# Kernel tuning notes

Hardware: AMD Instinct MI355X
Metric: run time of the kernel (lower is better)

Reference implementation:

```python
import jax, jax.numpy as jnp
import numpy as np

T, D, H = 2048, 2048, 16
DH = D // H


def setup_inputs() -> dict:
    key = jax.random.key(0)
    ks = jax.random.split(key, 9)
    s = 1.0 / np.sqrt(D)
    return {
        "x": jax.random.normal(ks[0], (T, D), jnp.float32),
        "Wq": jax.random.normal(ks[1], (D, D), jnp.float32) * s,
        "bq": jax.random.normal(ks[2], (D,), jnp.float32) * s,
        "Wk": jax.random.normal(ks[3], (D, D), jnp.float32) * s,
        "bk": jax.random.normal(ks[4], (D,), jnp.float32) * s,
        "Wv": jax.random.normal(ks[5], (D, D), jnp.float32) * s,
        "bv": jax.random.normal(ks[6], (D,), jnp.float32) * s,
        "Wo": jax.random.normal(ks[7], (D, D), jnp.float32) * s,
        "bo": jax.random.normal(ks[8], (D,), jnp.float32) * s,
    }


def reference(x, Wq, bq, Wk, bk, Wv, bv, Wo, bo):
    # torch Linear: y = x @ W.T + b; weights are [out, in]
    Q = (x @ Wq.T + bq).reshape(T, H, DH).transpose(1, 0, 2)  # [H, T, dh]
    K = (x @ Wk.T + bk).reshape(T, H, DH).transpose(1, 0, 2)
    V = (x @ Wv.T + bv).reshape(T, H, DH).transpose(1, 0, 2)
    scores = jnp.einsum("htd,hsd->hts", Q, K) / jnp.sqrt(jnp.float32(DH))
    causal = jnp.tril(jnp.ones((T, T), dtype=bool))  # True = keep
    scores = jnp.where(causal[None, :, :], scores, jnp.float32(-jnp.inf))
    P = jax.nn.softmax(scores, axis=-1)
    Y = jnp.einsum("hts,hsd->htd", P, V)  # [H, T, dh]
    Y = Y.transpose(1, 0, 2).reshape(T, D)
    return Y @ Wo.T + bo
```

## Files before the change

### kernel.cpp

```cpp
#include <hip/hip_runtime.h>
#include <hip/hip_fp16.h>
#include <math.h>

#define T_DIM 2048
#define D_DIM 2048
#define NHEAD 16
#define DHEAD 128

typedef _Float16 h8 __attribute__((ext_vector_type(8)));
typedef float v4f __attribute__((ext_vector_type(4)));
typedef unsigned short ush;

#define MFMAH(a, b, c) __builtin_amdgcn_mfma_f32_16x16x32_f16((a), (b), (c), 0, 0, 0)

__device__ __forceinline__ ush f2h(float f) {
    return __half_as_ushort(__float2half(f));
}
__device__ __forceinline__ unsigned pack2(ush a, ush b) {
    return (unsigned)a | ((unsigned)b << 16);
}

__device__ __forceinline__ void gload_lds16(const ush* g, ush* l) {
    __builtin_amdgcn_global_load_lds(
        (const __attribute__((address_space(1))) void*)g,
        (__attribute__((address_space(3))) void*)l, 16, 0, 0);
}

__device__ __forceinline__ void region_swizzle(int bid, int& m0, int& n0) {
    const int xcd = bid & 7;
    const int lg  = bid >> 3;
    const int mp  = ((xcd >> 2) << 3) + (lg >> 3);
    const int np  = ((xcd & 3) << 3) + (lg & 7);
    m0 = mp * 128;
    n0 = np * 64;
}

struct Cvt5Args { const float* s[5]; ush* d[5]; };

__global__ __launch_bounds__(256) void cvt5(Cvt5Args a)
{
    const int m = blockIdx.y;
    const float* X = a.s[m];
    ush* Dst = a.d[m];
    const int i = (blockIdx.x * 256 + threadIdx.x) * 8;
    const float4 p = *(const float4*)&X[i];
    const float4 q = *(const float4*)&X[i + 4];
    uint4 o;
    o.x = pack2(f2h(p.x), f2h(p.y));
    o.y = pack2(f2h(p.z), f2h(p.w));
    o.z = pack2(f2h(q.x), f2h(q.y));
    o.w = pack2(f2h(q.z), f2h(q.w));
    *(uint4*)&Dst[i] = o;
}

__global__ __launch_bounds__(256, 2) void gemm_qkv_f16(
    const ush* __restrict__ xf,
    const ush* __restrict__ Wqf, const ush* __restrict__ Wkf,
    const ush* __restrict__ Wvf,
    const float* __restrict__ bq, const float* __restrict__ bk,
    const float* __restrict__ bv, float qscale,
    ush* __restrict__ Qo, ush* __restrict__ Ko, ush* __restrict__ Vto)
{
    __shared__ ush As[128 * 64];
    __shared__ ush Bs[3][64 * 64];

    const int tid = threadIdx.x;
    const int l   = tid & 63;
    const int wid = tid >> 6;
    const int wm  = wid >> 1;
    const int wn  = wid & 1;
    const int cl  = l & 15;
    const int rg  = l >> 4;

    int m0, n0;
    region_swizzle(blockIdx.x, m0, n0);

    const ush* Wf[3] = {Wqf, Wkf, Wvf};

    v4f acc[3][4][2];
#pragma unroll
    for (int wg = 0; wg < 3; ++wg)
#pragma unroll
        for (int mf = 0; mf < 4; ++mf)
#pragma unroll
            for (int nf = 0; nf < 2; ++nf) acc[wg][mf][nf] = (v4f)0.f;

    for (int ks = 0; ks < D_DIM / 64; ++ks) {
        const int k0 = ks * 64;
        __syncthreads();
#pragma unroll
        for (int i = 0; i < 4; ++i) {
            const int p   = i * 256 + tid;
            const int row = p >> 3;
            const int lc  = (p & 7) ^ (row & 7);
            gload_lds16(&xf[(size_t)(m0 + row) * D_DIM + k0 + lc * 8], &As[p * 8]);
        }
#pragma unroll
        for (int i = 0; i < 2; ++i) {
            const int p   = i * 256 + tid;
            const int row = p >> 3;
            const int lc  = (p & 7) ^ (row & 7);
            const size_t off = (size_t)(n0 + row) * D_DIM + k0 + lc * 8;
#pragma unroll
            for (int wg = 0; wg < 3; ++wg)
                gload_lds16(&Wf[wg][off], &Bs[wg][p * 8]);
        }
        __syncthreads();

#pragma unroll
        for (int kf = 0; kf < 2; ++kf) {
            const int c = kf * 4 + rg;
            h8 a[4];
#pragma unroll
            for (int mf = 0; mf < 4; ++mf) {
                const int r = wm * 64 + mf * 16 + cl;
                a[mf] = *(const h8*)&As[r * 64 + ((c ^ (r & 7)) * 8)];
            }
#pragma unroll
            for (int wg = 0; wg < 3; ++wg) {
                h8 b[2];
#pragma unroll
                for (int nf = 0; nf < 2; ++nf) {
                    const int r = wn * 32 + nf * 16 + cl;
                    b[nf] = *(const h8*)&Bs[wg][r * 64 + ((c ^ (r & 7)) * 8)];
                }
#pragma unroll
                for (int mf = 0; mf < 4; ++mf)
#pragma unroll
                    for (int nf = 0; nf < 2; ++nf)
                        acc[wg][mf][nf] = MFMAH(a[mf], b[nf], acc[wg][mf][nf]);
            }
        }
    }

#pragma unroll
    for (int mf = 0; mf < 4; ++mf)
#pragma unroll
        for (int nf = 0; nf < 2; ++nf) {
            const int n  = n0 + wn * 32 + nf * 16 + cl;
            const int mb = m0 + wm * 64 + mf * 16 + rg * 4;
            const float bvq = bq[n], bvk = bk[n], bvv = bv[n];
#pragma unroll
            for (int j = 0; j < 4; ++j) {
                Qo[(size_t)(mb + j) * D_DIM + n] =
                    f2h((acc[0][mf][nf][j] + bvq) * qscale);
                Ko[(size_t)(mb + j) * D_DIM + n] =
                    f2h(acc[1][mf][nf][j] + bvk);
            }
            ushort4 pk;
            pk.x = f2h(acc[2][mf][nf][0] + bvv);
            pk.y = f2h(acc[2][mf][nf][1] + bvv);
            pk.z = f2h(acc[2][mf][nf][2] + bvv);
            pk.w = f2h(acc[2][mf][nf][3] + bvv);
            *(ushort4*)&Vto[(size_t)n * D_DIM + mb] = pk;
        }
}

__global__ __launch_bounds__(256, 2) void gemm_o_f16(
    const ush* __restrict__ Yf, const ush* __restrict__ Wof,
    const float* __restrict__ bo, float* __restrict__ out)
{
    __shared__ ush As[128 * 64];
    __shared__ ush Bs[64 * 64];

    const int tid = threadIdx.x;
    const int l   = tid & 63;
    const int wid = tid >> 6;
    const int wm  = wid >> 1;
    const int wn  = wid & 1;
    const int cl  = l & 15;
    const int rg  = l >> 4;

    int m0, n0;
    region_swizzle(blockIdx.x, m0, n0);

    v4f acc[4][2];
#pragma unroll
    for (int mf = 0; mf < 4; ++mf)
#pragma unroll
        for (int nf = 0; nf < 2; ++nf) acc[mf][nf] = (v4f)0.f;

    for (int ks = 0; ks < D_DIM / 64; ++ks) {
        const int k0 = ks * 64;
        __syncthreads();
#pragma unroll
        for (int i = 0; i < 4; ++i) {
            const int p   = i * 256 + tid;
            const int row = p >> 3;
            const int lc  = (p & 7) ^ (row & 7);
            gload_lds16(&Yf[(size_t)(m0 + row) * D_DIM + k0 + lc * 8], &As[p * 8]);
        }
#pragma unroll
        for (int i = 0; i < 2; ++i) {
            const int p   = i * 256 + tid;
            const int row = p >> 3;
            const int lc  = (p & 7) ^ (row & 7);
            gload_lds16(&Wof[(size_t)(n0 + row) * D_DIM + k0 + lc * 8], &Bs[p * 8]);
        }
        __syncthreads();

#pragma unroll
        for (int kf = 0; kf < 2; ++kf) {
            const int c = kf * 4 + rg;
            h8 a[4], b[2];
#pragma unroll
            for (int mf = 0; mf < 4; ++mf) {
                const int r = wm * 64 + mf * 16 + cl;
                a[mf] = *(const h8*)&As[r * 64 + ((c ^ (r & 7)) * 8)];
            }
#pragma unroll
            for (int nf = 0; nf < 2; ++nf) {
                const int r = wn * 32 + nf * 16 + cl;
                b[nf] = *(const h8*)&Bs[r * 64 + ((c ^ (r & 7)) * 8)];
            }
#pragma unroll
            for (int mf = 0; mf < 4; ++mf)
#pragma unroll
                for (int nf = 0; nf < 2; ++nf)
                    acc[mf][nf] = MFMAH(a[mf], b[nf], acc[mf][nf]);
        }
    }

#pragma unroll
    for (int mf = 0; mf < 4; ++mf)
#pragma unroll
        for (int nf = 0; nf < 2; ++nf) {
            const int n  = n0 + wn * 32 + nf * 16 + cl;
            const int mb = m0 + wm * 64 + mf * 16 + rg * 4;
            const float bv = bo[n];
#pragma unroll
            for (int j = 0; j < 4; ++j)
                out[(size_t)(mb + j) * D_DIM + n] = acc[mf][nf][j] + bv;
        }
}

__global__ __launch_bounds__(512, 4) void attn_fused(
    const ush* __restrict__ Qg, const ush* __restrict__ Kg,
    const ush* __restrict__ Vtg, ush* __restrict__ Yf)
{
    extern __shared__ char smem[];
    const int b   = blockIdx.x;
    const int h   = b & 15;
    const int qt  = (b < 256) ? (31 - (b >> 4)) : ((b >> 4) - 16);
    const int q0  = qt * 64;
    const int tid = threadIdx.x;
    const int l   = tid & 63;
    const int wid = tid >> 6;
    const int grp = wid >> 2;
    const int w   = wid & 3;
    const int cl  = l & 15;
    const int rg  = l >> 4;
    const int clx = cl & 7;
    const int tg  = tid & 255;

    char* gbase = smem + grp * 32768;
    ush* Ks = (ush*)gbase;
    ush* Vs = (ush*)(gbase + 16384);

    const int split = (qt + 2) >> 1;
    const int iters = split;
    const int t0    = grp ? split : 0;
    const int tcnt  = grp ? (qt + 1 - split) : split;

    const int qrow = q0 + w * 16 + cl;

    h8 qf[4];
#pragma unroll
    for (int kf = 0; kf < 4; ++kf)
        qf[kf] = *(const h8*)&Qg[(size_t)qrow * D_DIM + h * DHEAD + kf * 32 + rg * 8];

    v4f acc[8];
#pragma unroll
    for (int nf = 0; nf < 8; ++nf) acc[nf] = (v4f)0.f;
    float mrow = -INFINITY;
    float lsum = 0.f;

    auto stage = [&](int tile) {
#pragma unroll
        for (int i = 0; i < 4; ++i) {
            const int id = i * 256 + tg;
            const int kr = id >> 4, kc = id & 15;
            gload_lds16(&Kg[(size_t)(tile * 64 + kr) * D_DIM + h * DHEAD +
                            ((kc ^ (kr & 7)) * 8)], &Ks[id * 8]);
        }
#pragma unroll
        for (int i = 0; i < 4; ++i) {
            const int id = i * 256 + tg;
            const int vr = id >> 3, vc = id & 7;
            gload_lds16(&Vtg[(size_t)(h * DHEAD + vr) * D_DIM + tile * 64 +
                             ((vc ^ (vr & 7)) * 8)], &Vs[id * 8]);
        }
    };

    for (int t = 0; t < iters; ++t) {
        __syncthreads();
        if (t < tcnt) stage(t0 + t);
        __syncthreads();
        if (t < tcnt) {
            const int tile = t0 + t;

            v4f st[4];
#pragma unroll
            for (int n = 0; n < 4; ++n) st[n] = (v4f)0.f;
            __builtin_amdgcn_s_setprio(1);
#pragma unroll
            for (int kf = 0; kf < 4; ++kf) {
#pragma unroll
                for (int n = 0; n < 4; ++n) {
                    const h8 kfr = *(const h8*)&Ks[(n * 16 + cl) * 128 +
                                    (((kf * 4 + rg) ^ clx) * 8)];
                    st[n] = MFMAH(kfr, qf[kf], st[n]);
                }
            }
            __builtin_amdgcn_s_setprio(0);

            float sv[4][4];
            const bool dm = (tile == qt);
#pragma unroll
            for (int n = 0; n < 4; ++n)
#pragma unroll
                for (int jj = 0; jj < 4; ++jj) {
                    float v = st[n][jj];
                    if (dm && (tile * 64 + n * 16 + rg * 4 + jj > qrow))
                        v = -INFINITY;
                    sv[n][jj] = v;
                }
            float mx = sv[0][0];
#pragma unroll
            for (int n = 0; n < 4; ++n)
#pragma unroll
                for (int jj = 0; jj < 4; ++jj) mx = fmaxf(mx, sv[n][jj]);
            mx = fmaxf(mx, __shfl_xor(mx, 16));
            mx = fmaxf(mx, __shfl_xor(mx, 32));
            const float mnew = fmaxf(mrow, mx);

            uint2 pk[4];
            float rs = 0.f;
#pragma unroll
            for (int n = 0; n < 4; ++n) {
                float p0 = exp2f(sv[n][0] - mnew);
                float p1 = exp2f(sv[n][1] - mnew);
                float p2 = exp2f(sv[n][2] - mnew);
                float p3 = exp2f(sv[n][3] - mnew);
                rs += (p0 + p1) + (p2 + p3);
                pk[n].x = pack2(f2h(p0), f2h(p1));
                pk[n].y = pack2(f2h(p2), f2h(p3));
            }
            rs += __shfl_xor(rs, 16);
            rs += __shfl_xor(rs, 32);

            const float corr = exp2f(mrow - mnew);
            lsum = lsum * corr + rs;
            mrow = mnew;
#pragma unroll
            for (int nf = 0; nf < 8; ++nf) acc[nf] *= corr;

            const int s0 = cl + ((rg & 1) << 5);
            const int s1 = s0 + 16;
            const bool lo = (rg < 2);
            h8 pa[2];
#pragma unroll
            for (int kk = 0; kk < 2; ++kk) {
                union { uint4 u; h8 hv; } cv;
                const int xa = __shfl((int)pk[kk * 2].x, s0);
                const int xb = __shfl((int)pk[kk * 2 + 1].x, s0);
                const int ya = __shfl((int)pk[kk * 2].y, s0);
                const int yb = __shfl((int)pk[kk * 2 + 1].y, s0);
                const int za = __shfl((int)pk[kk * 2].x, s1);
                const int zb = __shfl((int)pk[kk * 2 + 1].x, s1);
                const int wa = __shfl((int)pk[kk * 2].y, s1);
                const int wb = __shfl((int)pk[kk * 2 + 1].y, s1);
                cv.u.x = (unsigned)(lo ? xa : xb);
                cv.u.y = (unsigned)(lo ? ya : yb);
                cv.u.z = (unsigned)(lo ? za : zb);
                cv.u.w = (unsigned)(lo ? wa : wb);
                pa[kk] = cv.hv;
            }

            __builtin_amdgcn_s_setprio(1);
#pragma unroll
            for (int nf = 0; nf < 8; ++nf) {
#pragma unroll
                for (int kk = 0; kk < 2; ++kk) {
                    const h8 vb = *(const h8*)&Vs[(nf * 16 + cl) * 64 +
                                   (((kk * 4 + rg) ^ clx) * 8)];
                    acc[nf] = MFMAH(vb, pa[kk], acc[nf]);
                }
            }
            __builtin_amdgcn_s_setprio(0);
        }
    }

    float* mAcc = (float*)smem;
    float* mML  = (float*)(smem + 33792);

    const int lr = w * 16 + cl;
    __syncthreads();
    if (grp == 1) {
#pragma unroll
        for (int nf = 0; nf < 8; ++nf)
            *(v4f*)&mAcc[lr * 132 + nf * 16 + rg * 4] = acc[nf];
        if (rg == 0) {
            mML[lr * 2]     = mrow;
            mML[lr * 2 + 1] = lsum;
        }
    }
    __syncthreads();
    if (grp == 0) {
        const float m1 = mML[lr * 2];
        const float l1 = mML[lr * 2 + 1];
        const float ms = fmaxf(mrow, m1);
        const float e0 = exp2f(mrow - ms);
        const float e1 = exp2f(m1 - ms);
        const float inv = 1.0f / (lsum * e0 + l1 * e1);
        const float s0 = e0 * inv, s1 = e1 * inv;
#pragma unroll
        for (int nf = 0; nf < 8; ++nf) {
            const v4f a1 = *(const v4f*)&mAcc[lr * 132 + nf * 16 + rg * 4];
            ushort4 ph;
            ph.x = f2h(acc[nf][0] * s0 + a1[0] * s1);
            ph.y = f2h(acc[nf][1] * s0 + a1[1] * s1);
            ph.z = f2h(acc[nf][2] * s0 + a1[2] * s1);
            ph.w = f2h(acc[nf][3] * s0 + a1[3] * s1);
            const size_t o = (size_t)(q0 + lr) * D_DIM + h * DHEAD + nf * 16 + rg * 4;
            *(ushort4*)&Yf[o] = ph;
        }
    }
}

extern "C" void kernel_launch(void* const* d_in, const int* in_sizes, int n_in,
                              void* d_out, int out_size, void* d_ws, size_t ws_size,
                              hipStream_t stream)
{
    const float* x  = (const float*)d_in[0];
    const float* Wq = (const float*)d_in[1];
    const float* bq = (const float*)d_in[2];
    const float* Wk = (const float*)d_in[3];
    const float* bk = (const float*)d_in[4];
    const float* Wv = (const float*)d_in[5];
    const float* bv = (const float*)d_in[6];
    const float* Wo = (const float*)d_in[7];
    const float* bo = (const float*)d_in[8];
    float* out = (float*)d_out;

    const size_t mat = (size_t)T_DIM * D_DIM;
    const float qscale = 0.08838834764831845f * 1.4426950408889634f;

    const int attn_lds = 65536;
    hipFuncSetAttribute((const void*)attn_fused,
                        hipFuncAttributeMaxDynamicSharedMemorySize, attn_lds);

    ush* xf   = (ush*)d_ws;
    ush* Qf   = xf  + mat;
    ush* Kf   = Qf  + mat;
    ush* Vtf  = Kf  + mat;
    ush* Wqf  = Vtf + mat;
    ush* Wkf  = Wqf + mat;
    ush* Wvf  = Wkf + mat;
    ush* Wof  = Wvf + mat;
    ush* Yf   = xf;

    Cvt5Args ca;
    ca.s[0] = x;  ca.d[0] = xf;
    ca.s[1] = Wq; ca.d[1] = Wqf;
    ca.s[2] = Wk; ca.d[2] = Wkf;
    ca.s[3] = Wv; ca.d[3] = Wvf;
    ca.s[4] = Wo; ca.d[4] = Wof;
    cvt5<<<dim3(mat / 2048, 5), 256, 0, stream>>>(ca);

    gemm_qkv_f16<<<512, 256, 0, stream>>>(
        xf, Wqf, Wkf, Wvf, bq, bk, bv, qscale, Qf, Kf, Vtf);

    attn_fused<<<512, 512, attn_lds, stream>>>(Qf, Kf, Vtf, Yf);

    gemm_o_f16<<<512, 256, 0, stream>>>(Yf, Wof, bo, out);
}
```

Baseline: 149.0 us.

## Remove split-KV intra-block parallelism from causal attention kernel

```diff
diff --git a/kernel.cpp b/kernel.cpp
--- a/kernel.cpp
+++ b/kernel.cpp
@@ -234,33 +234,23 @@
         }
 }
 
-__global__ __launch_bounds__(512, 4) void attn_fused(
+__global__ __launch_bounds__(256, 4) void attn_fused(
     const ush* __restrict__ Qg, const ush* __restrict__ Kg,
     const ush* __restrict__ Vtg, ush* __restrict__ Yf)
 {
-    extern __shared__ char smem[];
+    __shared__ ush Ks[64 * 128];
+    __shared__ ush Vs[128 * 64];
+
     const int b   = blockIdx.x;
     const int h   = b & 15;
-    const int qt  = (b < 256) ? (31 - (b >> 4)) : ((b >> 4) - 16);
+    const int qt  = 31 - (b >> 4);
     const int q0  = qt * 64;
     const int tid = threadIdx.x;
     const int l   = tid & 63;
-    const int wid = tid >> 6;
-    const int grp = wid >> 2;
-    const int w   = wid & 3;
+    const int w   = tid >> 6;
     const int cl  = l & 15;
     const int rg  = l >> 4;
     const int clx = cl & 7;
-    const int tg  = tid & 255;
-
-    char* gbase = smem + grp * 32768;
-    ush* Ks = (ush*)gbase;
-    ush* Vs = (ush*)(gbase + 16384);
-
-    const int split = (qt + 2) >> 1;
-    const int iters = split;
-    const int t0    = grp ? split : 0;
-    const int tcnt  = grp ? (qt + 1 - split) : split;
 
     const int qrow = q0 + w * 16 + cl;
 
@@ -278,153 +268,126 @@
     auto stage = [&](int tile) {
 #pragma unroll
         for (int i = 0; i < 4; ++i) {
-            const int id = i * 256 + tg;
+            const int id = i * 256 + tid;
             const int kr = id >> 4, kc = id & 15;
             gload_lds16(&Kg[(size_t)(tile * 64 + kr) * D_DIM + h * DHEAD +
                             ((kc ^ (kr & 7)) * 8)], &Ks[id * 8]);
         }
 #pragma unroll
         for (int i = 0; i < 4; ++i) {
-            const int id = i * 256 + tg;
+            const int id = i * 256 + tid;
             const int vr = id >> 3, vc = id & 7;
             gload_lds16(&Vtg[(size_t)(h * DHEAD + vr) * D_DIM + tile * 64 +
                              ((vc ^ (vr & 7)) * 8)], &Vs[id * 8]);
         }
     };
 
-    for (int t = 0; t < iters; ++t) {
-        __syncthreads();
-        if (t < tcnt) stage(t0 + t);
-        __syncthreads();
-        if (t < tcnt) {
-            const int tile = t0 + t;
-
-            v4f st[4];
-#pragma unroll
-            for (int n = 0; n < 4; ++n) st[n] = (v4f)0.f;
-            __builtin_amdgcn_s_setprio(1);
-#pragma unroll
-            for (int kf = 0; kf < 4; ++kf) {
-#pragma unroll
-                for (int n = 0; n < 4; ++n) {
-                    const h8 kfr = *(const h8*)&Ks[(n * 16 + cl) * 128 +
-                                    (((kf * 4 + rg) ^ clx) * 8)];
-                    st[n] = MFMAH(kfr, qf[kf], st[n]);
-                }
-            }
-            __builtin_amdgcn_s_setprio(0);
-
-            float sv[4][4];
-            const bool dm = (tile == qt);
-#pragma unroll
-            for (int n = 0; n < 4; ++n)
-#pragma unroll
-                for (int jj = 0; jj < 4; ++jj) {
-                    float v = st[n][jj];
-                    if (dm && (tile * 64 + n * 16 + rg * 4 + jj > qrow))
-                        v = -INFINITY;
-                    sv[n][jj] = v;
-                }
-            float mx = sv[0][0];
-#pragma unroll
-            for (int n = 0; n < 4; ++n)
-#pragma unroll
-                for (int jj = 0; jj < 4; ++jj) mx = fmaxf(mx, sv[n][jj]);
-            mx = fmaxf(mx, __shfl_xor(mx, 16));
-            mx = fmaxf(mx, __shfl_xor(mx, 32));
-            const float mnew = fmaxf(mrow, mx);
-
-            uint2 pk[4];
-            float rs = 0.f;
+    for (int t = 0; t <= qt; ++t) {
+        __syncthreads();
+        stage(t);
+        __syncthreads();
+
+        v4f st[4];
+#pragma unroll
+        for (int n = 0; n < 4; ++n) st[n] = (v4f)0.f;
+        __builtin_amdgcn_s_setprio(1);
+#pragma unroll
+        for (int kf = 0; kf < 4; ++kf) {
 #pragma unroll
             for (int n = 0; n < 4; ++n) {
-                float p0 = exp2f(sv[n][0] - mnew);
-                float p1 = exp2f(sv[n][1] - mnew);
-                float p2 = exp2f(sv[n][2] - mnew);
-                float p3 = exp2f(sv[n][3] - mnew);
-                rs += (p0 + p1) + (p2 + p3);
-                pk[n].x = pack2(f2h(p0), f2h(p1));
-                pk[n].y = pack2(f2h(p2), f2h(p3));
-            }
-            rs += __shfl_xor(rs, 16);
-            rs += __shfl_xor(rs, 32);
-
-            const float corr = exp2f(mrow - mnew);
-            lsum = lsum * corr + rs;
-            mrow = mnew;
-#pragma unroll
-            for (int nf = 0; nf < 8; ++nf) acc[nf] *= corr;
-
-            const int s0 = cl + ((rg & 1) << 5);
-            const int s1 = s0 + 16;
-            const bool lo = (rg < 2);
-            h8 pa[2];
+                const h8 kfr = *(const h8*)&Ks[(n * 16 + cl) * 128 +
+                                (((kf * 4 + rg) ^ clx) * 8)];
+                st[n] = MFMAH(kfr, qf[kf], st[n]);
+            }
+        }
+        __builtin_amdgcn_s_setprio(0);
+
+        float sv[4][4];
+        const bool dm = (t == qt);
+#pragma unroll
+        for (int n = 0; n < 4; ++n)
+#pragma unroll
+            for (int jj = 0; jj < 4; ++jj) {
+                float v = st[n][jj];
+                if (dm && (t * 64 + n * 16 + rg * 4 + jj > qrow))
+                    v = -INFINITY;
+                sv[n][jj] = v;
+            }
+        float mx = sv[0][0];
+#pragma unroll
+        for (int n = 0; n < 4; ++n)
+#pragma unroll
+            for (int jj = 0; jj < 4; ++jj) mx = fmaxf(mx, sv[n][jj]);
+        mx = fmaxf(mx, __shfl_xor(mx, 16));
+        mx = fmaxf(mx, __shfl_xor(mx, 32));
+        const float mnew = fmaxf(mrow, mx);
+
+        uint2 pk[4];
+        float rs = 0.f;
+#pragma unroll
+        for (int n = 0; n < 4; ++n) {
+            float p0 = exp2f(sv[n][0] - mnew);
+            float p1 = exp2f(sv[n][1] - mnew);
+            float p2 = exp2f(sv[n][2] - mnew);
+            float p3 = exp2f(sv[n][3] - mnew);
+            rs += (p0 + p1) + (p2 + p3);
+            pk[n].x = pack2(f2h(p0), f2h(p1));
+            pk[n].y = pack2(f2h(p2), f2h(p3));
+        }
+        rs += __shfl_xor(rs, 16);
+        rs += __shfl_xor(rs, 32);
+
+        const float corr = exp2f(mrow - mnew);
+        lsum = lsum * corr + rs;
+        mrow = mnew;
+#pragma unroll
+        for (int nf = 0; nf < 8; ++nf) acc[nf] *= corr;
+
+        const int s0 = cl + ((rg & 1) << 5);
+        const int s1 = s0 + 16;
+        const bool lo = (rg < 2);
+        h8 pa[2];
+#pragma unroll
+        for (int kk = 0; kk < 2; ++kk) {
+            union { uint4 u; h8 hv; } cv;
+            const int xa = __shfl((int)pk[kk * 2].x, s0);
+            const int xb = __shfl((int)pk[kk * 2 + 1].x, s0);
+            const int ya = __shfl((int)pk[kk * 2].y, s0);
+            const int yb = __shfl((int)pk[kk * 2 + 1].y, s0);
+            const int za = __shfl((int)pk[kk * 2].x, s1);
+            const int zb = __shfl((int)pk[kk * 2 + 1].x, s1);
+            const int wa = __shfl((int)pk[kk * 2].y, s1);
+            const int wb = __shfl((int)pk[kk * 2 + 1].y, s1);
+            cv.u.x = (unsigned)(lo ? xa : xb);
+            cv.u.y = (unsigned)(lo ? ya : yb);
+            cv.u.z = (unsigned)(lo ? za : zb);
+            cv.u.w = (unsigned)(lo ? wa : wb);
+            pa[kk] = cv.hv;
+        }
+
+        __builtin_amdgcn_s_setprio(1);
+#pragma unroll
+        for (int nf = 0; nf < 8; ++nf) {
 #pragma unroll
             for (int kk = 0; kk < 2; ++kk) {
-                union { uint4 u; h8 hv; } cv;
-                const int xa = __shfl((int)pk[kk * 2].x, s0);
-                const int xb = __shfl((int)pk[kk * 2 + 1].x, s0);
-                const int ya = __shfl((int)pk[kk * 2].y, s0);
-                const int yb = __shfl((int)pk[kk * 2 + 1].y, s0);
-                const int za = __shfl((int)pk[kk * 2].x, s1);
-                const int zb = __shfl((int)pk[kk * 2 + 1].x, s1);
-                const int wa = __shfl((int)pk[kk * 2].y, s1);
-                const int wb = __shfl((int)pk[kk * 2 + 1].y, s1);
-                cv.u.x = (unsigned)(lo ? xa : xb);
-                cv.u.y = (unsigned)(lo ? ya : yb);
-                cv.u.z = (unsigned)(lo ? za : zb);
-                cv.u.w = (unsigned)(lo ? wa : wb);
-                pa[kk] = cv.hv;
-            }
-
-            __builtin_amdgcn_s_setprio(1);
-#pragma unroll
-            for (int nf = 0; nf < 8; ++nf) {
-#pragma unroll
-                for (int kk = 0; kk < 2; ++kk) {
-                    const h8 vb = *(const h8*)&Vs[(nf * 16 + cl) * 64 +
-                                   (((kk * 4 + rg) ^ clx) * 8)];
-                    acc[nf] = MFMAH(vb, pa[kk], acc[nf]);
-                }
-            }
-            __builtin_amdgcn_s_setprio(0);
-        }
+                const h8 vb = *(const h8*)&Vs[(nf * 16 + cl) * 64 +
+                               (((kk * 4 + rg) ^ clx) * 8)];
+                acc[nf] = MFMAH(vb, pa[kk], acc[nf]);
+            }
+        }
+        __builtin_amdgcn_s_setprio(0);
     }
 
-    float* mAcc = (float*)smem;
-    float* mML  = (float*)(smem + 33792);
-
-    const int lr = w * 16 + cl;
-    __syncthreads();
-    if (grp == 1) {
-#pragma unroll
-        for (int nf = 0; nf < 8; ++nf)
-            *(v4f*)&mAcc[lr * 132 + nf * 16 + rg * 4] = acc[nf];
-        if (rg == 0) {
-            mML[lr * 2]     = mrow;
-            mML[lr * 2 + 1] = lsum;
-        }
-    }
-    __syncthreads();
-    if (grp == 0) {
-        const float m1 = mML[lr * 2];
-        const float l1 = mML[lr * 2 + 1];
-        const float ms = fmaxf(mrow, m1);
-        const float e0 = exp2f(mrow - ms);
-        const float e1 = exp2f(m1 - ms);
-        const float inv = 1.0f / (lsum * e0 + l1 * e1);
-        const float s0 = e0 * inv, s1 = e1 * inv;
-#pragma unroll
-        for (int nf = 0; nf < 8; ++nf) {
-            const v4f a1 = *(const v4f*)&mAcc[lr * 132 + nf * 16 + rg * 4];
-            ushort4 ph;
-            ph.x = f2h(acc[nf][0] * s0 + a1[0] * s1);
-            ph.y = f2h(acc[nf][1] * s0 + a1[1] * s1);
-            ph.z = f2h(acc[nf][2] * s0 + a1[2] * s1);
-            ph.w = f2h(acc[nf][3] * s0 + a1[3] * s1);
-            const size_t o = (size_t)(q0 + lr) * D_DIM + h * DHEAD + nf * 16 + rg * 4;
-            *(ushort4*)&Yf[o] = ph;
-        }
+    const float inv = 1.0f / lsum;
+#pragma unroll
+    for (int nf = 0; nf < 8; ++nf) {
+        ushort4 ph;
+        ph.x = f2h(acc[nf][0] * inv);
+        ph.y = f2h(acc[nf][1] * inv);
+        ph.z = f2h(acc[nf][2] * inv);
+        ph.w = f2h(acc[nf][3] * inv);
+        const size_t o = (size_t)qrow * D_DIM + h * DHEAD + nf * 16 + rg * 4;
+        *(ushort4*)&Yf[o] = ph;
     }
 }
 
@@ -446,10 +409,6 @@
     const size_t mat = (size_t)T_DIM * D_DIM;
     const float qscale = 0.08838834764831845f * 1.4426950408889634f;
 
-    const int attn_lds = 65536;
-    hipFuncSetAttribute((const void*)attn_fused,
-                        hipFuncAttributeMaxDynamicSharedMemorySize, attn_lds);
-
     ush* xf   = (ush*)d_ws;
     ush* Qf   = xf  + mat;
     ush* Kf   = Qf  + mat;
@@ -471,7 +430,7 @@
     gemm_qkv_f16<<<512, 256, 0, stream>>>(
         xf, Wqf, Wkf, Wvf, bq, bk, bv, qscale, Qf, Kf, Vtf);
 
-    attn_fused<<<512, 512, attn_lds, stream>>>(Qf, Kf, Vtf, Yf);
+    attn_fused<<<512, 256, 0, stream>>>(Qf, Kf, Vtf, Yf);
 
     gemm_o_f16<<<512, 256, 0, stream>>>(Yf, Wof, bo, out);
 }
```

Measured after the change: 170.3 us. 1.14x slower.
